# Kernel optimization log

Measured on AMD Instinct MI355X. Metric: run time of the kernel, lower is better.

## Reference

```python
import jax, jax.numpy as jnp
import numpy as np
from math import sqrt

B, S, E, H = 2, 2048, 1024, 16

def setup_inputs() -> dict:
    key = jax.random.key(0)
    k1, k2, k3, k4, k5 = jax.random.split(key, 5)
    bound_in = 1.0 / sqrt(E)
    return {
        "inputs": jax.random.normal(k1, (B, S, E), dtype=jnp.float32),
        "W_in": jax.random.uniform(k2, (3 * E, E), dtype=jnp.float32, minval=-bound_in, maxval=bound_in),
        "b_in": jax.random.uniform(k3, (3 * E,), dtype=jnp.float32, minval=-bound_in, maxval=bound_in),
        "W_out": jax.random.uniform(k4, (E, E), dtype=jnp.float32, minval=-bound_in, maxval=bound_in),
        "b_out": jax.random.uniform(k5, (E,), dtype=jnp.float32, minval=-bound_in, maxval=bound_in),
    }

def reference(inputs, W_in, b_in, W_out, b_out):
    # Eval-mode forward (dropout is identity when not training).
    b, s, e = inputs.shape
    hd = e // H
    qkv = jnp.einsum('bse,fe->bsf', inputs, W_in) + b_in  # [B,S,3E]
    q, k, v = jnp.split(qkv, 3, axis=-1)
    # [B,S,E] -> [B,H,S,hd]
    to_heads = lambda t: t.reshape(b, s, H, hd).transpose(0, 2, 1, 3)
    q, k, v = to_heads(q), to_heads(k), to_heads(v)
    scores = jnp.einsum('bhqd,bhkd->bhqk', q, k) / jnp.sqrt(jnp.float32(hd))
    causal = jnp.tril(jnp.ones((s, s), dtype=bool))
    scores = jnp.where(causal, scores, -jnp.inf)
    attn = jax.nn.softmax(scores, axis=-1)  # stable max-subtract softmax, same math
    out = jnp.einsum('bhqk,bhkd->bhqd', attn, v)  # [B,H,S,hd]
    out = out.transpose(0, 2, 1, 3).reshape(b, s, e)
    return jnp.einsum('bse,fe->bsf', out, W_out) + b_out
```

## Files before the change

kernel.cpp:

```cpp
#include <hip/hip_runtime.h>
#include <hip/hip_bf16.h>
#include <stdint.h>

#define SS 2048
#define EE 1024
#define HH 16
#define HD 64

#define QSCALE 0.1803368801111137f

typedef __attribute__((ext_vector_type(8))) short short8;
typedef __attribute__((ext_vector_type(4))) float f32x4;

__device__ __forceinline__ short f2bf(float f) {
  union { float f; uint32_t u; } x; x.f = f;
  uint32_t r = x.u + 0x7fffu + ((x.u >> 16) & 1u);
  return (short)(r >> 16);
}

__device__ __forceinline__ uint32_t pk_bf16(float a, float b) {
#if __has_builtin(__builtin_amdgcn_cvt_pk_bf16_f32)
  typedef __attribute__((ext_vector_type(2))) __bf16 bf16x2_t;
  union { bf16x2_t v; uint32_t u; } x;
  x.v = __builtin_amdgcn_cvt_pk_bf16_f32(a, b);
  return x.u;
#else
  return (uint32_t)(uint16_t)f2bf(a) | ((uint32_t)(uint16_t)f2bf(b) << 16);
#endif
}

__device__ __forceinline__ void async_cp16(const void* g, void* l) {
  __builtin_amdgcn_global_load_lds((const __attribute__((address_space(1))) void*)g,
                                   (__attribute__((address_space(3))) void*)l, 16, 0, 0);
}

#define N4_X  1048576
#define N4_W1 786432
#define N4_W2 262144
__global__ __launch_bounds__(256) void cvt_all(
    const float* __restrict__ x, const float* __restrict__ w1,
    const float* __restrict__ w2,
    short* __restrict__ xb, short* __restrict__ w1b, short* __restrict__ w2b)
{
  int i = blockIdx.x * 256 + threadIdx.x;
  const float* src; short* dst; int off;
  if (i < N4_X)            { src = x;  dst = xb;  off = i; }
  else if (i < N4_X+N4_W1) { src = w1; dst = w1b; off = i - N4_X; }
  else                     { src = w2; dst = w2b; off = i - N4_X - N4_W1; }
  float4 v = *(const float4*)&src[(size_t)off * 4];
  uint2 pk;
  pk.x = pk_bf16(v.x, v.y);
  pk.y = pk_bf16(v.z, v.w);
  *(uint2*)&dst[(size_t)off * 4] = pk;
}

template<int MODE>
__global__ __launch_bounds__(256) void gemm_db(
    const short* __restrict__ A, const short* __restrict__ Bw,
    const float* __restrict__ bias,
    float* __restrict__ C,
    short* __restrict__ qw, short* __restrict__ kw, short* __restrict__ vw,
    int M, int N, int K)
{
  __shared__ short smem[(MODE == 1) ? 17408 : 16384];
  const int tid = threadIdx.x;
  const int lane = tid & 63;
  const int wv = tid >> 6;
  const int wm = (wv >> 1) * 64;
  const int wn = (wv & 1) * 64;
  const int t = lane >> 4;
  const int lr = lane & 15;
  const int bm = blockIdx.y * 128;
  const int bn = blockIdx.x * 128;

  f32x4 acc[4][4];
  #pragma unroll
  for (int i = 0; i < 4; ++i)
    #pragma unroll
    for (int j = 0; j < 4; ++j) acc[i][j] = (f32x4){0.f, 0.f, 0.f, 0.f};

  auto stage = [&](int buf, int k0) {
    short* sA = smem + buf * 8192;
    short* sB = smem + buf * 8192 + 4096;
    #pragma unroll
    for (int it = 0; it < 2; ++it) {
      int c = it * 256 + wv * 64 + lane;
      int row = c >> 2;
      int ch = (c & 3) * 8;
      async_cp16(&A[(size_t)(bm + row) * K + k0 + ch],
                 (char*)sA + (size_t)(it * 256 + wv * 64) * 16);
      async_cp16(&Bw[(size_t)(bn + row) * K + k0 + ch],
                 (char*)sB + (size_t)(it * 256 + wv * 64) * 16);
    }
  };

  const int nk = K >> 5;
  stage(0, 0);
  __syncthreads();

  for (int k = 0; k < nk; ++k) {
    if (k + 1 < nk) stage((k + 1) & 1, (k + 1) << 5);
    const short* cA = smem + (k & 1) * 8192;
    const short* cB = smem + (k & 1) * 8192 + 4096;
    short8 af[4], bfr[4];
    #pragma unroll
    for (int i = 0; i < 4; ++i) af[i] = *(const short8*)&cA[(wm + i*16 + lr)*32 + t*8];
    #pragma unroll
    for (int j = 0; j < 4; ++j) bfr[j] = *(const short8*)&cB[(wn + j*16 + lr)*32 + t*8];
    #pragma unroll
    for (int i = 0; i < 4; ++i)
      #pragma unroll
      for (int j = 0; j < 4; ++j)
        acc[i][j] = __builtin_amdgcn_mfma_f32_16x16x32_bf16(af[i], bfr[j], acc[i][j], 0, 0, 0);
    __syncthreads();
  }

  if (MODE == 1 && bn >= 2048) {
    short* vx = smem;
    #pragma unroll
    for (int i = 0; i < 4; ++i) {
      int row0 = wm + i*16 + t*4;
      #pragma unroll
      for (int j = 0; j < 4; ++j) {
        int cl = wn + j*16 + lr;
        float bv = bias[bn + cl];
        #pragma unroll
        for (int r = 0; r < 4; ++r)
          vx[cl*136 + row0 + r] = f2bf(acc[i][j][r] + bv);
      }
    }
    __syncthreads();
    int h0 = (bn - 2048) >> 6;
    int b_ = bm >> 11;
    int s0 = bm & 2047;
    #pragma unroll
    for (int it = 0; it < 8; ++it) {
      int cc = it * 256 + tid;
      int cl = cc >> 4;
      int ck = cc & 15;
      int h = h0 + (cl >> 6);
      int d = cl & 63;
      *(uint4*)&vw[((size_t)(b_*HH + h)*HD + d)*SS + s0 + ck*8] =
          *(const uint4*)&vx[cl*136 + ck*8];
    }
    return;
  }

  #pragma unroll
  for (int i = 0; i < 4; ++i) {
    int row0 = bm + wm + i*16 + t*4;
    #pragma unroll
    for (int j = 0; j < 4; ++j) {
      int col = bn + wn + j*16 + lr;
      float bv = bias[col];
      #pragma unroll
      for (int r = 0; r < 4; ++r) {
        float v = acc[i][j][r] + bv;
        int rr = row0 + r;
        if (MODE == 0) {
          C[(size_t)rr * N + col] = v;
        } else {
          int e = col & 1023;
          int h = e >> 6, d = e & 63;
          int b_ = rr >> 11, s = rr & 2047;
          if (col < 1024)
            qw[((size_t)(b_*HH + h)*SS + s)*HD + d] = f2bf(v * QSCALE);
          else
            kw[((size_t)(b_*HH + h)*SS + s)*HD + d] = f2bf(v);
        }
      }
    }
  }
}

template<int MODE, typename TA>
__global__ __launch_bounds__(256) void gemm_bt(
    const TA* __restrict__ A, const float* __restrict__ Bw,
    const float* __restrict__ bias,
    float* __restrict__ C,
    short* __restrict__ qw, short* __restrict__ kw, short* __restrict__ vw,
    int M, int N, int K)
{
  __shared__ short sA[128*32];
  __shared__ short sB[128*32];
  const int tid = threadIdx.x;
  const int lane = tid & 63;
  const int wv = tid >> 6;
  const int wm = (wv >> 1) * 64;
  const int wn = (wv & 1) * 64;
  const int t = lane >> 4;
  const int lr = lane & 15;
  const int bm = blockIdx.y * 128;
  const int bn = blockIdx.x * 128;

  f32x4 acc[4][4];
  #pragma unroll
  for (int i = 0; i < 4; ++i)
    #pragma unroll
    for (int j = 0; j < 4; ++j) acc[i][j] = (f32x4){0.f, 0.f, 0.f, 0.f};

  for (int k0 = 0; k0 < K; k0 += 32) {
    __syncthreads();
    if constexpr (sizeof(TA) == 4) {
      #pragma unroll
      for (int it = 0; it < 4; ++it) {
        int c = it * 256 + tid;
        int row = c >> 3, ch = (c & 7) * 4;
        float4 va = *(const float4*)&A[(size_t)(bm + row)*K + k0 + ch];
        uint2 pk; pk.x = pk_bf16(va.x, va.y); pk.y = pk_bf16(va.z, va.w);
        *(uint2*)&sA[row*32 + ch] = pk;
      }
    } else {
      #pragma unroll
      for (int it = 0; it < 2; ++it) {
        int c = it * 256 + tid;
        int row = c >> 2, ch = (c & 3) * 8;
        *(uint4*)&sA[row*32 + ch] = *(const uint4*)&A[(size_t)(bm + row)*K + k0 + ch];
      }
    }
    #pragma unroll
    for (int it = 0; it < 4; ++it) {
      int c = it * 256 + tid;
      int row = c >> 3, ch = (c & 7) * 4;
      float4 vb = *(const float4*)&Bw[(size_t)(bn + row)*K + k0 + ch];
      uint2 pk; pk.x = pk_bf16(vb.x, vb.y); pk.y = pk_bf16(vb.z, vb.w);
      *(uint2*)&sB[row*32 + ch] = pk;
    }
    __syncthreads();
    short8 af[4], bfr[4];
    #pragma unroll
    for (int i = 0; i < 4; ++i) af[i] = *(const short8*)&sA[(wm + i*16 + lr)*32 + t*8];
    #pragma unroll
    for (int j = 0; j < 4; ++j) bfr[j] = *(const short8*)&sB[(wn + j*16 + lr)*32 + t*8];
    #pragma unroll
    for (int i = 0; i < 4; ++i)
      #pragma unroll
      for (int j = 0; j < 4; ++j)
        acc[i][j] = __builtin_amdgcn_mfma_f32_16x16x32_bf16(af[i], bfr[j], acc[i][j], 0, 0, 0);
  }

  #pragma unroll
  for (int i = 0; i < 4; ++i) {
    int row0 = bm + wm + i*16 + t*4;
    #pragma unroll
    for (int j = 0; j < 4; ++j) {
      int col = bn + wn + j*16 + lr;
      float bv = bias[col];
      #pragma unroll
      for (int r = 0; r < 4; ++r) {
        float v = acc[i][j][r] + bv;
        int rr = row0 + r;
        if (MODE == 0) {
          C[(size_t)rr * N + col] = v;
        } else {
          int which = col >> 10;
          int e = col & 1023;
          int h = e >> 6, d = e & 63;
          int b_ = rr >> 11, s = rr & 2047;
          if (which == 0)
            qw[((size_t)(b_*HH + h)*SS + s)*HD + d] = f2bf(v * QSCALE);
          else if (which == 1)
            kw[((size_t)(b_*HH + h)*SS + s)*HD + d] = f2bf(v);
          else
            vw[((size_t)(b_*HH + h)*HD + d)*SS + s] = f2bf(v);
        }
      }
    }
  }
}

__global__ __launch_bounds__(512) void attn_kernel(
    const short* __restrict__ Q, const short* __restrict__ K,
    const short* __restrict__ Vt, short* __restrict__ O)
{
  __shared__ short sK[2][128*64];
  __shared__ short sV[2][64*128];
  __shared__ short sP[8][16*64];
  const int tid = threadIdx.x;
  const int lane = tid & 63;
  const int w = tid >> 6;
  const int t = lane >> 4;
  const int lr = lane & 15;
  const int blk = blockIdx.x;
  const int qt = (blk < 256) ? (blk >> 5) : (15 - ((blk - 256) >> 5));
  const int bh = blk & 31;
  const int b = bh >> 4, h = bh & 15;
  const short* Qb = Q  + (size_t)bh * SS * HD;
  const short* Kb = K  + (size_t)bh * SS * HD;
  const short* Vb = Vt + (size_t)bh * HD * SS;
  const int qrow0 = qt * 128 + w * 16;
  short* sPw = sP[w];

  auto stage = [&](int buf, int kb) {
    #pragma unroll
    for (int it2 = 0; it2 < 2; ++it2) {
      int s = it2 * 512 + tid;
      int krow = s >> 3;
      int kcc = (s & 7) ^ (krow & 7);
      async_cp16(&Kb[(size_t)(kb + krow) * HD + kcc * 8],
                 (char*)sK[buf] + (size_t)(it2 * 512 + w * 64) * 16);
      int d = s >> 4;
      int vcc = (s & 15) ^ (d & 15);
      async_cp16(&Vb[(size_t)d * SS + kb + vcc * 8],
                 (char*)sV[buf] + (size_t)(it2 * 512 + w * 64) * 16);
    }
  };

  short8 qf[2];
  #pragma unroll
  for (int st = 0; st < 2; ++st)
    qf[st] = *(const short8*)&Qb[(size_t)(qrow0 + lr) * HD + st*32 + t*8];

  f32x4 o[4];
  #pragma unroll
  for (int jd = 0; jd < 4; ++jd) o[jd] = (f32x4){0.f, 0.f, 0.f, 0.f};
  float l = 0.f;

  const int niter = qt + 1;
  stage(0, 0);
  __syncthreads();
  int cur = 0;

  #pragma unroll 1
  for (int it = 0; it < niter; ++it) {
    const int kb = it * 128;
    if (it + 1 < niter) stage(cur ^ 1, kb + 128);
    const short* sKc = sK[cur];
    const short* sVc = sV[cur];

    f32x4 sc[8];
    #pragma unroll
    for (int c = 0; c < 8; ++c) sc[c] = (f32x4){0.f,0.f,0.f,0.f};
    #pragma unroll
    for (int c = 0; c < 8; ++c) {
      int krow = c*16 + lr;
      #pragma unroll
      for (int st = 0; st < 2; ++st) {
        int slot = krow*8 + ((st*4 + t) ^ (krow & 7));
        short8 kf = *(const short8*)&sKc[slot*8];
        sc[c] = __builtin_amdgcn_mfma_f32_16x16x32_bf16(kf, qf[st], sc[c], 0, 0, 0);
      }
    }

    if (it == niter - 1) {
      int qg = qrow0 + lr;
      #pragma unroll
      for (int c = 0; c < 8; ++c)
        #pragma unroll
        for (int r = 0; r < 4; ++r)
          if (kb + c*16 + t*4 + r > qg) sc[c][r] = -1e30f;
    }

    float rs = 0.f;
    #pragma unroll
    for (int c = 0; c < 8; ++c)
      #pragma unroll
      for (int r = 0; r < 4; ++r) {
        sc[c][r] = exp2f(sc[c][r]);
        rs += sc[c][r];
      }
    rs += __shfl_xor(rs, 16);
    rs += __shfl_xor(rs, 32);
    l += rs;

    #pragma unroll
    for (int hf = 0; hf < 2; ++hf) {
      #pragma unroll
      for (int c2 = 0; c2 < 4; ++c2) {
        int c = hf*4 + c2;
        uint2 pk2;
        pk2.x = pk_bf16(sc[c][0], sc[c][1]);
        pk2.y = pk_bf16(sc[c][2], sc[c][3]);
        int chunk = 2*c2 + (t >> 1);
        *(uint2*)&sPw[lr*64 + ((chunk ^ (lr & 7)) * 8) + (t & 1) * 4] = pk2;
      }
      #pragma unroll
      for (int fl = 0; fl < 2; ++fl) {
        int chunk = 4*fl + t;
        short8 pf = *(const short8*)&sPw[lr*64 + ((chunk ^ (lr & 7)) * 8)];
        int f = hf*2 + fl;
        #pragma unroll
        for (int jd = 0; jd < 4; ++jd) {
          int d = jd*16 + lr;
          int vslot = d*16 + ((f*4 + t) ^ (d & 15));
          short8 vf = *(const short8*)&sVc[vslot*8];
          o[jd] = __builtin_amdgcn_mfma_f32_16x16x32_bf16(vf, pf, o[jd], 0, 0, 0);
        }
      }
    }

    __syncthreads();
    cur ^= 1;
  }

  float linv = 1.0f / l;
  size_t rowoff = ((size_t)(b * SS + qrow0 + lr)) * EE + h * HD;
  #pragma unroll
  for (int jd = 0; jd < 4; ++jd) {
    uint2 pw;
    pw.x = pk_bf16(o[jd][0] * linv, o[jd][1] * linv);
    pw.y = pk_bf16(o[jd][2] * linv, o[jd][3] * linv);
    *(uint2*)&O[rowoff + jd*16 + t*4] = pw;
  }
}

extern "C" void kernel_launch(void* const* d_in, const int* in_sizes, int n_in,
                              void* d_out, int out_size, void* d_ws, size_t ws_size,
                              hipStream_t stream) {
  const float* X     = (const float*)d_in[0];
  const float* W_in  = (const float*)d_in[1];
  const float* b_in  = (const float*)d_in[2];
  const float* W_out = (const float*)d_in[3];
  const float* b_out = (const float*)d_in[4];
  float* out = (float*)d_out;

  char* ws = (char*)d_ws;
  const size_t MB = 1024 * 1024;
  const int M = 2 * SS;

  if (ws_size >= 48 * MB) {
    short* Xb   = (short*)(ws);
    short* Wb1  = (short*)(ws + 8  * MB);
    short* Wb2  = (short*)(ws + 14 * MB);
    short* q_ws = (short*)(ws + 16 * MB);
    short* k_ws = (short*)(ws + 24 * MB);
    short* v_ws = (short*)(ws + 32 * MB);
    short* attn = (short*)(ws + 40 * MB);

    cvt_all<<<8192, 256, 0, stream>>>(X, W_in, W_out, Xb, Wb1, Wb2);
    gemm_db<1><<<dim3(24, 32), 256, 0, stream>>>(
        Xb, Wb1, b_in, nullptr, q_ws, k_ws, v_ws, M, 3 * EE, EE);
    attn_kernel<<<dim3(512), 512, 0, stream>>>(q_ws, k_ws, v_ws, attn);
    gemm_db<0><<<dim3(8, 32), 256, 0, stream>>>(
        attn, Wb2, b_out, out, nullptr, nullptr, nullptr, M, EE, EE);
  } else {
    short* q_ws = (short*)(ws);
    short* k_ws = (short*)(ws + 8  * MB);
    short* v_ws = (short*)(ws + 16 * MB);
    short* attn = (short*)(ws + 24 * MB);

    gemm_bt<1, float><<<dim3(24, 32), 256, 0, stream>>>(
        X, W_in, b_in, nullptr, q_ws, k_ws, v_ws, M, 3 * EE, EE);
    attn_kernel<<<dim3(512), 512, 0, stream>>>(q_ws, k_ws, v_ws, attn);
    gemm_bt<0, short><<<dim3(8, 32), 256, 0, stream>>>(
        attn, W_out, b_out, out, nullptr, nullptr, nullptr, M, EE, EE);
  }
}
```

Baseline: 194.6 us.

## Process two 16-row query groups per wave in attention, halve block threads

The attention kernel now runs 4 waves per block instead of 8. Each wave handles 32 query rows as two 16-row groups, so every K and V fragment read from shared memory feeds two MFMAs. The aim is to halve LDS fragment traffic per unit of compute and raise MFMA density. In exchange each wave holds more accumulator registers and has fewer waves to hide latency, and each thread now issues twice as many staging copies.

Result: slower. 199.1 us (+2.3%).

```diff
diff --git a/kernel.cpp b/kernel.cpp
--- a/kernel.cpp
+++ b/kernel.cpp
@@ -269,13 +269,13 @@
   }
 }
 
-__global__ __launch_bounds__(512) void attn_kernel(
+__global__ __launch_bounds__(256) void attn_kernel(
     const short* __restrict__ Q, const short* __restrict__ K,
     const short* __restrict__ Vt, short* __restrict__ O)
 {
   __shared__ short sK[2][128*64];
   __shared__ short sV[2][64*128];
-  __shared__ short sP[8][16*64];
+  __shared__ short sP[4][16*64];
   const int tid = threadIdx.x;
   const int lane = tid & 63;
   const int w = tid >> 6;
@@ -288,33 +288,38 @@
   const short* Qb = Q  + (size_t)bh * SS * HD;
   const short* Kb = K  + (size_t)bh * SS * HD;
   const short* Vb = Vt + (size_t)bh * HD * SS;
-  const int qrow0 = qt * 128 + w * 16;
+  const int qrow0 = qt * 128 + w * 32;
   short* sPw = sP[w];
 
   auto stage = [&](int buf, int kb) {
     #pragma unroll
-    for (int it2 = 0; it2 < 2; ++it2) {
-      int s = it2 * 512 + tid;
+    for (int it2 = 0; it2 < 4; ++it2) {
+      int s = it2 * 256 + tid;
       int krow = s >> 3;
       int kcc = (s & 7) ^ (krow & 7);
       async_cp16(&Kb[(size_t)(kb + krow) * HD + kcc * 8],
-                 (char*)sK[buf] + (size_t)(it2 * 512 + w * 64) * 16);
+                 (char*)sK[buf] + (size_t)(it2 * 256 + w * 64) * 16);
       int d = s >> 4;
       int vcc = (s & 15) ^ (d & 15);
       async_cp16(&Vb[(size_t)d * SS + kb + vcc * 8],
-                 (char*)sV[buf] + (size_t)(it2 * 512 + w * 64) * 16);
+                 (char*)sV[buf] + (size_t)(it2 * 256 + w * 64) * 16);
     }
   };
 
-  short8 qf[2];
-  #pragma unroll
-  for (int st = 0; st < 2; ++st)
-    qf[st] = *(const short8*)&Qb[(size_t)(qrow0 + lr) * HD + st*32 + t*8];
-
-  f32x4 o[4];
-  #pragma unroll
-  for (int jd = 0; jd < 4; ++jd) o[jd] = (f32x4){0.f, 0.f, 0.f, 0.f};
-  float l = 0.f;
+  short8 qf[2][2];
+  #pragma unroll
+  for (int g = 0; g < 2; ++g)
+    #pragma unroll
+    for (int st = 0; st < 2; ++st)
+      qf[g][st] = *(const short8*)&Qb[(size_t)(qrow0 + g*16 + lr) * HD + st*32 + t*8];
+
+  f32x4 o0[4], o1[4];
+  #pragma unroll
+  for (int jd = 0; jd < 4; ++jd) {
+    o0[jd] = (f32x4){0.f, 0.f, 0.f, 0.f};
+    o1[jd] = (f32x4){0.f, 0.f, 0.f, 0.f};
+  }
+  float l0 = 0.f, l1 = 0.f;
 
   const int niter = qt + 1;
   stage(0, 0);
@@ -328,9 +333,12 @@
     const short* sKc = sK[cur];
     const short* sVc = sV[cur];
 
-    f32x4 sc[8];
-    #pragma unroll
-    for (int c = 0; c < 8; ++c) sc[c] = (f32x4){0.f,0.f,0.f,0.f};
+    f32x4 sc0[8], sc1[8];
+    #pragma unroll
+    for (int c = 0; c < 8; ++c) {
+      sc0[c] = (f32x4){0.f,0.f,0.f,0.f};
+      sc1[c] = (f32x4){0.f,0.f,0.f,0.f};
+    }
     #pragma unroll
     for (int c = 0; c < 8; ++c) {
       int krow = c*16 + lr;
@@ -338,53 +346,82 @@
       for (int st = 0; st < 2; ++st) {
         int slot = krow*8 + ((st*4 + t) ^ (krow & 7));
         short8 kf = *(const short8*)&sKc[slot*8];
-        sc[c] = __builtin_amdgcn_mfma_f32_16x16x32_bf16(kf, qf[st], sc[c], 0, 0, 0);
+        sc0[c] = __builtin_amdgcn_mfma_f32_16x16x32_bf16(kf, qf[0][st], sc0[c], 0, 0, 0);
+        sc1[c] = __builtin_amdgcn_mfma_f32_16x16x32_bf16(kf, qf[1][st], sc1[c], 0, 0, 0);
       }
     }
 
     if (it == niter - 1) {
-      int qg = qrow0 + lr;
+      int qg0 = qrow0 + lr;
+      int qg1 = qg0 + 16;
       #pragma unroll
       for (int c = 0; c < 8; ++c)
         #pragma unroll
-        for (int r = 0; r < 4; ++r)
-          if (kb + c*16 + t*4 + r > qg) sc[c][r] = -1e30f;
-    }
-
-    float rs = 0.f;
+        for (int r = 0; r < 4; ++r) {
+          int kv = kb + c*16 + t*4 + r;
+          if (kv > qg0) sc0[c][r] = -1e30f;
+          if (kv > qg1) sc1[c][r] = -1e30f;
+        }
+    }
+
+    float rs0 = 0.f, rs1 = 0.f;
     #pragma unroll
     for (int c = 0; c < 8; ++c)
       #pragma unroll
       for (int r = 0; r < 4; ++r) {
-        sc[c][r] = exp2f(sc[c][r]);
-        rs += sc[c][r];
-      }
-    rs += __shfl_xor(rs, 16);
-    rs += __shfl_xor(rs, 32);
-    l += rs;
+        sc0[c][r] = exp2f(sc0[c][r]);
+        rs0 += sc0[c][r];
+        sc1[c][r] = exp2f(sc1[c][r]);
+        rs1 += sc1[c][r];
+      }
+    rs0 += __shfl_xor(rs0, 16);
+    rs0 += __shfl_xor(rs0, 32);
+    rs1 += __shfl_xor(rs1, 16);
+    rs1 += __shfl_xor(rs1, 32);
+    l0 += rs0;
+    l1 += rs1;
 
     #pragma unroll
     for (int hf = 0; hf < 2; ++hf) {
+      short8 pf0[2], pf1[2];
       #pragma unroll
       for (int c2 = 0; c2 < 4; ++c2) {
         int c = hf*4 + c2;
         uint2 pk2;
-        pk2.x = pk_bf16(sc[c][0], sc[c][1]);
-        pk2.y = pk_bf16(sc[c][2], sc[c][3]);
+        pk2.x = pk_bf16(sc0[c][0], sc0[c][1]);
+        pk2.y = pk_bf16(sc0[c][2], sc0[c][3]);
         int chunk = 2*c2 + (t >> 1);
         *(uint2*)&sPw[lr*64 + ((chunk ^ (lr & 7)) * 8) + (t & 1) * 4] = pk2;
       }
       #pragma unroll
       for (int fl = 0; fl < 2; ++fl) {
         int chunk = 4*fl + t;
-        short8 pf = *(const short8*)&sPw[lr*64 + ((chunk ^ (lr & 7)) * 8)];
+        pf0[fl] = *(const short8*)&sPw[lr*64 + ((chunk ^ (lr & 7)) * 8)];
+      }
+      #pragma unroll
+      for (int c2 = 0; c2 < 4; ++c2) {
+        int c = hf*4 + c2;
+        uint2 pk2;
+        pk2.x = pk_bf16(sc1[c][0], sc1[c][1]);
+        pk2.y = pk_bf16(sc1[c][2], sc1[c][3]);
+        int chunk = 2*c2 + (t >> 1);
+        *(uint2*)&sPw[lr*64 + ((chunk ^ (lr & 7)) * 8) + (t & 1) * 4] = pk2;
+      }
+      #pragma unroll
+      for (int fl = 0; fl < 2; ++fl) {
+        int chunk = 4*fl + t;
+        pf1[fl] = *(const short8*)&sPw[lr*64 + ((chunk ^ (lr & 7)) * 8)];
+      }
+      #pragma unroll
+      for (int fl = 0; fl < 2; ++fl) {
         int f = hf*2 + fl;
         #pragma unroll
         for (int jd = 0; jd < 4; ++jd) {
           int d = jd*16 + lr;
           int vslot = d*16 + ((f*4 + t) ^ (d & 15));
           short8 vf = *(const short8*)&sVc[vslot*8];
-          o[jd] = __builtin_amdgcn_mfma_f32_16x16x32_bf16(vf, pf, o[jd], 0, 0, 0);
+          o0[jd] = __builtin_amdgcn_mfma_f32_16x16x32_bf16(vf, pf0[fl], o0[jd], 0, 0, 0);
+          o1[jd] = __builtin_amdgcn_mfma_f32_16x16x32_bf16(vf, pf1[fl], o1[jd], 0, 0, 0);
         }
       }
     }
@@ -393,14 +430,19 @@
     cur ^= 1;
   }
 
-  float linv = 1.0f / l;
-  size_t rowoff = ((size_t)(b * SS + qrow0 + lr)) * EE + h * HD;
+  float linv0 = 1.0f / l0;
+  float linv1 = 1.0f / l1;
+  size_t rowoff0 = ((size_t)(b * SS + qrow0 + lr)) * EE + h * HD;
+  size_t rowoff1 = rowoff0 + (size_t)16 * EE;
   #pragma unroll
   for (int jd = 0; jd < 4; ++jd) {
     uint2 pw;
-    pw.x = pk_bf16(o[jd][0] * linv, o[jd][1] * linv);
-    pw.y = pk_bf16(o[jd][2] * linv, o[jd][3] * linv);
-    *(uint2*)&O[rowoff + jd*16 + t*4] = pw;
+    pw.x = pk_bf16(o0[jd][0] * linv0, o0[jd][1] * linv0);
+    pw.y = pk_bf16(o0[jd][2] * linv0, o0[jd][3] * linv0);
+    *(uint2*)&O[rowoff0 + jd*16 + t*4] = pw;
+    pw.x = pk_bf16(o1[jd][0] * linv1, o1[jd][1] * linv1);
+    pw.y = pk_bf16(o1[jd][2] * linv1, o1[jd][3] * linv1);
+    *(uint2*)&O[rowoff1 + jd*16 + t*4] = pw;
   }
 }
 
@@ -430,7 +472,7 @@
     cvt_all<<<8192, 256, 0, stream>>>(X, W_in, W_out, Xb, Wb1, Wb2);
     gemm_db<1><<<dim3(24, 32), 256, 0, stream>>>(
         Xb, Wb1, b_in, nullptr, q_ws, k_ws, v_ws, M, 3 * EE, EE);
-    attn_kernel<<<dim3(512), 512, 0, stream>>>(q_ws, k_ws, v_ws, attn);
+    attn_kernel<<<dim3(512), 256, 0, stream>>>(q_ws, k_ws, v_ws, attn);
     gemm_db<0><<<dim3(8, 32), 256, 0, stream>>>(
         attn, Wb2, b_out, out, nullptr, nullptr, nullptr, M, EE, EE);
   } else {
@@ -441,7 +483,7 @@
 
     gemm_bt<1, float><<<dim3(24, 32), 256, 0, stream>>>(
         X, W_in, b_in, nullptr, q_ws, k_ws, v_ws, M, 3 * EE, EE);
-    attn_kernel<<<dim3(512), 512, 0, stream>>>(q_ws, k_ws, v_ws, attn);
+    attn_kernel<<<dim3(512), 256, 0, stream>>>(q_ws, k_ws, v_ws, attn);
     gemm_bt<0, short><<<dim3(8, 32), 256, 0, stream>>>(
         attn, W_out, b_out, out, nullptr, nullptr, nullptr, M, EE, EE);
   }
```
